# Kernel tuning notes

Hardware: AMD Instinct MI355X
Metric: run time of the kernel (lower is better)

Reference implementation:

```python
import jax, jax.numpy as jnp
import numpy as np
from jax import lax

B, CIN, COUT, K, S, P, H, W = 8, 128, 256, 3, 1, 1, 64, 64


def setup_inputs() -> dict:
    key = jax.random.key(0)
    k1, k2, k3, k4, k5 = jax.random.split(key, 5)
    fan_off = CIN * K * K
    fan_dc = CIN * K * K
    return {
        "x": jax.random.normal(k1, (B, CIN, H, W), dtype=jnp.float32),
        # offset-predicting conv: Conv2d(CIN, 2*K*K, K, S, P, padding_mode='reflect')
        "w_off": jax.random.normal(k2, (2 * K * K, CIN, K, K), dtype=jnp.float32) / np.sqrt(fan_off),
        "b_off": jax.random.normal(k3, (2 * K * K,), dtype=jnp.float32) * 0.01,
        # deformable conv weights: DeformConv2d(CIN, COUT, K, S, P)
        "w_dc": jax.random.normal(k4, (COUT, CIN, K, K), dtype=jnp.float32) / np.sqrt(fan_dc),
        "b_dc": jax.random.normal(k5, (COUT,), dtype=jnp.float32) * 0.01,
    }


def _reflect_conv(x, w, b, stride, pad):
    # Conv2d with reflect padding
    xp = jnp.pad(x, ((0, 0), (0, 0), (pad, pad), (pad, pad)), mode="reflect")
    y = lax.conv_general_dilated(xp, w, (stride, stride), "VALID",
                                 dimension_numbers=("NCHW", "OIHW", "NCHW"))
    return y + b[None, :, None, None]


def _deform_conv(x, offset, w, b, k, stride, pad):
    # torchvision DeformConv2d (v1, no mask, 1 offset group)
    Bn, C, Hi, Wi = x.shape
    Ho, Wo = offset.shape[2], offset.shape[3]
    KK = k * k
    # offset layout: [B, 2*KK, Ho, Wo], interleaved (dy, dx) per kernel position
    off = offset.reshape(Bn, KK, 2, Ho, Wo)
    hb = jnp.arange(Ho, dtype=x.dtype) * stride - pad          # base rows
    wb = jnp.arange(Wo, dtype=x.dtype) * stride - pad          # base cols
    ki, kj = jnp.meshgrid(jnp.arange(k, dtype=x.dtype), jnp.arange(k, dtype=x.dtype), indexing="ij")
    ki, kj = ki.reshape(KK), kj.reshape(KK)
    # sampling locations [B, KK, Ho, Wo]
    py = off[:, :, 0] + hb[None, None, :, None] + ki[None, :, None, None]
    px = off[:, :, 1] + wb[None, None, None, :] + kj[None, :, None, None]
    y0 = jnp.floor(py)
    x0 = jnp.floor(px)
    dy = (py - y0).reshape(Bn, 1, -1)
    dx = (px - x0).reshape(Bn, 1, -1)
    y0i = y0.astype(jnp.int32)
    x0i = x0.astype(jnp.int32)
    xf = x.reshape(Bn, C, Hi * Wi)

    def gather(yi, xi):
        valid = (yi >= 0) & (yi < Hi) & (xi >= 0) & (xi < Wi)
        yc = jnp.clip(yi, 0, Hi - 1)
        xc = jnp.clip(xi, 0, Wi - 1)
        idx = (yc * Wi + xc).reshape(Bn, -1)                   # [B, KK*Ho*Wo]
        g = jax.vmap(lambda xb, ib: xb[:, ib])(xf, idx)        # [B, C, KK*Ho*Wo]
        return g * valid.reshape(Bn, 1, -1).astype(x.dtype)

    v00 = gather(y0i, x0i)
    v01 = gather(y0i, x0i + 1)
    v10 = gather(y0i + 1, x0i)
    v11 = gather(y0i + 1, x0i + 1)
    vals = (v00 * (1 - dy) * (1 - dx) + v01 * (1 - dy) * dx
            + v10 * dy * (1 - dx) + v11 * dy * dx)             # [B, C, KK*Ho*Wo]
    cols = vals.reshape(Bn, C, KK, Ho * Wo)
    out = jnp.einsum("bckl,ock->bol", cols, w.reshape(-1, C, KK))
    out = out + b[None, :, None]
    return out.reshape(Bn, -1, Ho, Wo)


def reference(x, w_off, b_off, w_dc, b_dc):
    x_offset = _reflect_conv(x, w_off, b_off, S, P)            # [B, 2*K*K, Ho, Wo]
    # torch.chunk followed by torch.concat is an identity on the offset tensor
    return _deform_conv(x, x_offset, w_dc, b_dc, K, S, P)
```

## Files before the change

### kernel.cpp

```cpp
#include <hip/hip_runtime.h>
#include <hip/hip_fp16.h>

typedef unsigned short u16;
typedef unsigned int   u32;
typedef u32   u32x2  __attribute__((ext_vector_type(2)));
typedef u32   u32x4  __attribute__((ext_vector_type(4)));
typedef short short8 __attribute__((ext_vector_type(8)));
typedef float f32x4  __attribute__((ext_vector_type(4)));
typedef _Float16 half8 __attribute__((ext_vector_type(8)));

__device__ __forceinline__ u16 f2h(float f) { return __half_as_ushort(__float2half(f)); }
__device__ __forceinline__ f32x4 mfma16(short8 a, short8 b, f32x4 c) {
  return __builtin_amdgcn_mfma_f32_16x16x32_f16(
      __builtin_bit_cast(half8, a), __builtin_bit_cast(half8, b), c, 0, 0, 0);
}
__device__ __forceinline__ __half2 h2cast(u32 u) { return __builtin_bit_cast(__half2, u); }
__device__ __forceinline__ int refl(int v) { return v < 0 ? -v : (v > 63 ? 126 - v : v); }

__global__ __launch_bounds__(256) void prep_fused(const float* __restrict__ x,
                                                  const float* __restrict__ w_dc,
                                                  const float* __restrict__ w_off,
                                                  u16* __restrict__ xh,
                                                  u16* __restrict__ Wl2,
                                                  u16* __restrict__ Wol2) {
  int bid = blockIdx.x;
  int tid = threadIdx.x;
  if (bid < 512) {
    __shared__ float tile[128][65];
    int swz = (bid & 7) * 64 + (bid >> 3);
    int b = swz >> 6, h = swz & 63;
    for (int i = 0; i < 32; ++i) {
      int c = (tid >> 6) + i * 4;
      int w = tid & 63;
      tile[c][w] = x[(((size_t)b * 128 + c) * 64 + h) * 64 + w];
    }
    __syncthreads();
    u16* dst = xh + ((size_t)(b * 64 + h) * 64) * 128;
    for (int j = 0; j < 32; ++j) {
      int c = tid & 127;
      int w = (tid >> 7) + 2 * j;
      dst[w * 128 + c] = f2h(tile[c][w]);
    }
  } else {
    int idx = (bid - 512) * 256 + tid;
    if (idx < 294912) {
      int e = idx & 7, lane = (idx >> 3) & 63, ks = (idx >> 9) & 3;
      int mt = (idx >> 11) & 15, kk = idx >> 15;
      int o = mt * 16 + (lane & 15), c = ks * 32 + (lane >> 4) * 8 + e;
      Wl2[idx] = f2h(w_dc[(o * 128 + c) * 9 + kk]);
    } else {
      int i2 = idx - 294912;
      int e = i2 & 7, lane = (i2 >> 3) & 63, ks = (i2 >> 9) & 3;
      int mt = (i2 >> 11) & 1, kk = i2 >> 12;
      int co = mt * 16 + (lane & 15), c = ks * 32 + (lane >> 4) * 8 + e;
      Wol2[i2] = (co < 18) ? f2h(w_off[(co * 128 + c) * 9 + kk]) : (u16)0;
    }
  }
}

__device__ __forceinline__ void make_entry_lds(u32x4* __restrict__ tbl, int kk,
                                               int ho, int wo, float offy, float offx) {
  int ki = kk / 3, kj = kk - ki * 3;
  float py = offy + (float)(ho + ki - 1);
  float px = offx + (float)(wo + kj - 1);
  float fy0 = floorf(py), fx0 = floorf(px);
  int y0 = (int)fy0, x0 = (int)fx0;
  float fy = py - fy0, fx = px - fx0;
  float w11 = fy * fx, w10 = fy - w11, w01 = fx - w11, w00 = 1.f - fy - fx + w11;
  bool iy0 = (y0 >= 0) & (y0 < 64), iy1 = (y0 >= -1) & (y0 < 63);
  bool ix0 = (x0 >= 0) & (x0 < 64), ix1 = (x0 >= -1) & (x0 < 63);
  int y0c = min(max(y0, 0), 63), x0c = min(max(x0, 0), 63);
  u32 addr00 = (u32)((y0c * 64 + x0c) * 128);
  u32 dx = (x0 >= 0 && x0 < 63) ? 128u : 0u;
  u32 dy = (y0 >= 0 && y0 < 63) ? 8192u : 0u;
  u32 wA = (u32)f2h((iy0 && ix0) ? w00 : 0.f) | ((u32)f2h((iy0 && ix1) ? w01 : 0.f) << 16);
  u32 wB = (u32)f2h((iy1 && ix0) ? w10 : 0.f) | ((u32)f2h((iy1 && ix1) ? w11 : 0.f) << 16);
  u32x4 ent; ent.x = addr00; ent.y = dx | (dy << 16); ent.z = wA; ent.w = wB;
  tbl[kk * 64 + wo] = ent;
}

__global__ __launch_bounds__(512, 4) void deform_fused(
    const u16* __restrict__ xh, const u16* __restrict__ Wl2,
    const u16* __restrict__ Wol2, const float* __restrict__ b_off,
    const float* __restrict__ b_dc, float* __restrict__ out) {
  union SMU {
    u16 slab[3][64][128];
    struct { u16 cols[2][64][128]; u32x4 tbl[576]; } pb;
  };
  __shared__ SMU sm;
  int bid = blockIdx.x;
  int b = bid & 7, ho = bid >> 3;
  int tid = threadIdx.x, lane = tid & 63, wv = tid >> 6;
  int ln15 = lane & 15, kg = lane >> 4;
  const u16* xb = xh + (size_t)b * 524288;

  {
    u32x4 st[6];
#pragma unroll
    for (int i = 0; i < 6; ++i) {
      int T = tid + i * 512;
      int r = T >> 10, w = (T >> 4) & 63, cb = (T & 15) * 8;
      int hr = refl(ho + r - 1);
      st[i] = *(const u32x4*)(xb + (hr * 64 + w) * 128 + cb);
    }
#pragma unroll
    for (int i = 0; i < 6; ++i) {
      int T = tid + i * 512;
      int r = T >> 10, w = (T >> 4) & 63, cb = (T & 15) * 8;
      *(u32x4*)&sm.slab[r][w][cb ^ ((w & 7) << 3)] = st[i];
    }
  }
  __syncthreads();

  int mtA = wv & 1, ntA = wv >> 1;
  int lq = ntA * 16 + ln15;
  f32x4 oacc = {0.f, 0.f, 0.f, 0.f};
  __builtin_amdgcn_s_setprio(1);
#pragma unroll
  for (int kk = 0; kk < 9; ++kk) {
    int ki = kk / 3, kj = kk - ki * 3;
    int j = refl(lq + kj - 1);
    const u16* wb = Wol2 + ((kk * 2 + mtA) * 4) * 512 + lane * 8;
    int sbj = (j & 7) << 3;
#pragma unroll
    for (int ks = 0; ks < 4; ++ks) {
      short8 af = *(const short8*)(wb + ks * 512);
      short8 bf = *(const short8*)&sm.slab[ki][j][(ks * 32 + kg * 8) ^ sbj];
      oacc = mfma16(af, bf, oacc);
    }
  }
  __builtin_amdgcn_s_setprio(0);
  __syncthreads();

  if (mtA == 0) {
    int kkA = 2 * kg, kkB = 2 * kg + 1;
    make_entry_lds(sm.pb.tbl, kkA, ho, lq, oacc[0] + b_off[2 * kkA], oacc[1] + b_off[2 * kkA + 1]);
    make_entry_lds(sm.pb.tbl, kkB, ho, lq, oacc[2] + b_off[2 * kkB], oacc[3] + b_off[2 * kkB + 1]);
  } else if (kg == 0) {
    make_entry_lds(sm.pb.tbl, 8, ho, lq, oacc[0] + b_off[16], oacc[1] + b_off[17]);
  }
  __syncthreads();

  if (wv >= 4) {
    int pt = tid & 255;
    int tl = pt >> 4;
    int tcl = (pt & 15) * 8;
    int swzc = tcl ^ ((tl & 7) << 3);

    u32x4 gv[4][4];
    u32 gwA[4], gwB[4];
    auto gissue = [&](int g) {
#pragma unroll
      for (int i = 0; i < 4; ++i) {
        int l = tl + i * 16;
        u32x4 e = sm.pb.tbl[g * 64 + l];
        gwA[i] = e.z; gwB[i] = e.w;
        const u16* p = xb + e.x + tcl;
        u32 dxv = e.y & 0xffffu, dyv = e.y >> 16;
        gv[i][0] = *(const u32x4*)p;
        gv[i][1] = *(const u32x4*)(p + dxv);
        gv[i][2] = *(const u32x4*)(p + dyv);
        gv[i][3] = *(const u32x4*)(p + dyv + dxv);
      }
    };
    auto gwrite = [&](int dbuf) {
#pragma unroll
      for (int i = 0; i < 4; ++i) {
        int l = tl + i * 16;
        __half2 wA = h2cast(gwA[i]), wB = h2cast(gwB[i]);
        __half2 w00 = __half2half2(wA.x), w01 = __half2half2(wA.y);
        __half2 w10 = __half2half2(wB.x), w11 = __half2half2(wB.y);
        u32x4 pv;
#pragma unroll
        for (int wd = 0; wd < 4; ++wd) {
          __half2 r = __hmul2(h2cast(gv[i][0][wd]), w00);
          r = __hfma2(h2cast(gv[i][1][wd]), w01, r);
          r = __hfma2(h2cast(gv[i][2][wd]), w10, r);
          r = __hfma2(h2cast(gv[i][3][wd]), w11, r);
          pv[wd] = __builtin_bit_cast(u32, r);
        }
        *(u32x4*)&sm.pb.cols[dbuf][l][swzc] = pv;
      }
    };

    gissue(0); gwrite(0);
    gissue(1);
    __syncthreads();
    for (int kk = 0; kk < 9; ++kk) {
      int cur = kk & 1;
      if (kk < 8) gwrite(cur ^ 1);
      if (kk < 7) gissue(kk + 2);
      __syncthreads();
    }
  } else {
    f32x4 acc[4][4];
#pragma unroll
    for (int m = 0; m < 4; ++m)
#pragma unroll
      for (int n = 0; n < 4; ++n) acc[m][n] = (f32x4){0.f, 0.f, 0.f, 0.f};

    int swzb = (ln15 & 7) << 3;
    __syncthreads();
    for (int kk = 0; kk < 9; ++kk) {
      int cur = kk & 1;
      const u16* wb = Wl2 + (size_t)kk * 32768 + lane * 8;
      short8 ac[4], an[4];
#pragma unroll
      for (int m = 0; m < 4; ++m)
        ac[m] = *(const short8*)(wb + (size_t)((wv * 4 + m) * 4) * 512);
#pragma unroll
      for (int ks = 0; ks < 4; ++ks) {
        if (ks < 3) {
#pragma unroll
          for (int m = 0; m < 4; ++m)
            an[m] = *(const short8*)(wb + (size_t)((wv * 4 + m) * 4 + ks + 1) * 512);
        }
        __builtin_amdgcn_s_setprio(1);
#pragma unroll
        for (int nt = 0; nt < 4; ++nt) {
          short8 bf = *(const short8*)&sm.pb.cols[cur][nt * 16 + ln15][(ks * 32 + kg * 8) ^ swzb];
#pragma unroll
          for (int m = 0; m < 4; ++m)
            acc[m][nt] = mfma16(ac[m], bf, acc[m][nt]);
        }
        __builtin_amdgcn_s_setprio(0);
        if (ks < 3) {
#pragma unroll
          for (int m = 0; m < 4; ++m) ac[m] = an[m];
        }
      }
      __syncthreads();
    }

#pragma unroll
    for (int m = 0; m < 4; ++m) {
#pragma unroll
      for (int r = 0; r < 4; ++r) {
        int o = wv * 64 + m * 16 + kg * 4 + r;
        float bias = b_dc[o];
        size_t base = ((size_t)(b * 256 + o)) * 4096 + ho * 64;
#pragma unroll
        for (int nt = 0; nt < 4; ++nt) {
          out[base + nt * 16 + ln15] = acc[m][nt][r] + bias;
        }
      }
    }
  }
}

extern "C" void kernel_launch(void* const* d_in, const int* in_sizes, int n_in,
                              void* d_out, int out_size, void* d_ws, size_t ws_size,
                              hipStream_t stream) {
  const float* x     = (const float*)d_in[0];
  const float* w_off = (const float*)d_in[1];
  const float* b_off = (const float*)d_in[2];
  const float* w_dc  = (const float*)d_in[3];
  const float* b_dc  = (const float*)d_in[4];
  float* out = (float*)d_out;
  char* ws = (char*)d_ws;
  u16* xh   = (u16*)ws;
  u16* Wl2  = (u16*)(ws + 8388608);
  u16* Wol2 = (u16*)(ws + 8388608 + 589824);
  prep_fused  <<<dim3(1808), dim3(256), 0, stream>>>(x, w_dc, w_off, xh, Wl2, Wol2);
  deform_fused<<<dim3(512),  dim3(512), 0, stream>>>(xh, Wl2, Wol2, b_off, b_dc, out);
}
```

Baseline: 45.74 us.

## Split each output row into two 32-column halves to double block count

Each block now handles a 32-wide half of an output row instead of a full 64-wide row, so the grid doubles to 1024 blocks. The LDS slab shrinks to a 36-column halo window, the column and table buffers halve, and launch bounds ask for higher occupancy. The offset-conv MFMA work is restricted to four waves, and the GEMM drops its A-fragment prefetch and priority hints. This aims to fill more CUs and overlap more work, at the cost of reloading deform weights from global twice as often per row, plus a redundant halo load.

```diff
diff --git a/kernel.cpp b/kernel.cpp
--- a/kernel.cpp
+++ b/kernel.cpp
@@ -59,7 +59,8 @@
 }
 
 __device__ __forceinline__ void make_entry_lds(u32x4* __restrict__ tbl, int kk,
-                                               int ho, int wo, float offy, float offx) {
+                                               int ho, int wo, int lql,
+                                               float offy, float offx) {
   int ki = kk / 3, kj = kk - ki * 3;
   float py = offy + (float)(ho + ki - 1);
   float px = offx + (float)(wo + kj - 1);
@@ -76,84 +77,92 @@
   u32 wA = (u32)f2h((iy0 && ix0) ? w00 : 0.f) | ((u32)f2h((iy0 && ix1) ? w01 : 0.f) << 16);
   u32 wB = (u32)f2h((iy1 && ix0) ? w10 : 0.f) | ((u32)f2h((iy1 && ix1) ? w11 : 0.f) << 16);
   u32x4 ent; ent.x = addr00; ent.y = dx | (dy << 16); ent.z = wA; ent.w = wB;
-  tbl[kk * 64 + wo] = ent;
-}
-
-__global__ __launch_bounds__(512, 4) void deform_fused(
+  tbl[kk * 32 + lql] = ent;
+}
+
+__global__ __launch_bounds__(512, 8) void deform_fused(
     const u16* __restrict__ xh, const u16* __restrict__ Wl2,
     const u16* __restrict__ Wol2, const float* __restrict__ b_off,
     const float* __restrict__ b_dc, float* __restrict__ out) {
-  union SMU {
-    u16 slab[3][64][128];
-    struct { u16 cols[2][64][128]; u32x4 tbl[576]; } pb;
-  };
-  __shared__ SMU sm;
+  __shared__ union SMU {
+    u16 slab[3][36][128];
+    u16 cols[2][32][128];
+  } sm;
+  __shared__ u32x4 tbl[288];
+
   int bid = blockIdx.x;
-  int b = bid & 7, ho = bid >> 3;
+  int b = bid & 7;
+  int ho = (bid >> 3) & 63;
+  int l0 = (bid >> 9) * 32;
   int tid = threadIdx.x, lane = tid & 63, wv = tid >> 6;
   int ln15 = lane & 15, kg = lane >> 4;
   const u16* xb = xh + (size_t)b * 524288;
 
   {
-    u32x4 st[6];
-#pragma unroll
-    for (int i = 0; i < 6; ++i) {
+    u32x4 st[4];
+#pragma unroll
+    for (int i = 0; i < 4; ++i) {
       int T = tid + i * 512;
-      int r = T >> 10, w = (T >> 4) & 63, cb = (T & 15) * 8;
-      int hr = refl(ho + r - 1);
-      st[i] = *(const u32x4*)(xb + (hr * 64 + w) * 128 + cb);
-    }
-#pragma unroll
-    for (int i = 0; i < 6; ++i) {
+      if (T < 1728) {
+        int r = T / 576, rem = T - r * 576;
+        int j = rem >> 4, cb = (rem & 15) * 8;
+        int hr = refl(ho + r - 1);
+        int w = refl(l0 + j - 1);
+        st[i] = *(const u32x4*)(xb + (hr * 64 + w) * 128 + cb);
+      }
+    }
+#pragma unroll
+    for (int i = 0; i < 4; ++i) {
       int T = tid + i * 512;
-      int r = T >> 10, w = (T >> 4) & 63, cb = (T & 15) * 8;
-      *(u32x4*)&sm.slab[r][w][cb ^ ((w & 7) << 3)] = st[i];
+      if (T < 1728) {
+        int r = T / 576, rem = T - r * 576;
+        int j = rem >> 4, cb = (rem & 15) * 8;
+        *(u32x4*)&sm.slab[r][j][cb ^ ((j & 7) << 3)] = st[i];
+      }
     }
   }
   __syncthreads();
 
-  int mtA = wv & 1, ntA = wv >> 1;
-  int lq = ntA * 16 + ln15;
-  f32x4 oacc = {0.f, 0.f, 0.f, 0.f};
-  __builtin_amdgcn_s_setprio(1);
-#pragma unroll
-  for (int kk = 0; kk < 9; ++kk) {
-    int ki = kk / 3, kj = kk - ki * 3;
-    int j = refl(lq + kj - 1);
-    const u16* wb = Wol2 + ((kk * 2 + mtA) * 4) * 512 + lane * 8;
-    int sbj = (j & 7) << 3;
-#pragma unroll
-    for (int ks = 0; ks < 4; ++ks) {
-      short8 af = *(const short8*)(wb + ks * 512);
-      short8 bf = *(const short8*)&sm.slab[ki][j][(ks * 32 + kg * 8) ^ sbj];
-      oacc = mfma16(af, bf, oacc);
-    }
-  }
-  __builtin_amdgcn_s_setprio(0);
-  __syncthreads();
-
-  if (mtA == 0) {
-    int kkA = 2 * kg, kkB = 2 * kg + 1;
-    make_entry_lds(sm.pb.tbl, kkA, ho, lq, oacc[0] + b_off[2 * kkA], oacc[1] + b_off[2 * kkA + 1]);
-    make_entry_lds(sm.pb.tbl, kkB, ho, lq, oacc[2] + b_off[2 * kkB], oacc[3] + b_off[2 * kkB + 1]);
-  } else if (kg == 0) {
-    make_entry_lds(sm.pb.tbl, 8, ho, lq, oacc[0] + b_off[16], oacc[1] + b_off[17]);
+  if (wv < 4) {
+    int mtA = wv & 1, ntq = wv >> 1;
+    int lql = ntq * 16 + ln15;
+    f32x4 oacc = {0.f, 0.f, 0.f, 0.f};
+#pragma unroll
+    for (int kk = 0; kk < 9; ++kk) {
+      int ki = kk / 3, kj = kk - ki * 3;
+      int j = lql + kj;
+      int sbj = (j & 7) << 3;
+      const u16* wb = Wol2 + ((kk * 2 + mtA) * 4) * 512 + lane * 8;
+#pragma unroll
+      for (int ks = 0; ks < 4; ++ks) {
+        short8 af = *(const short8*)(wb + ks * 512);
+        short8 bf = *(const short8*)&sm.slab[ki][j][(ks * 32 + kg * 8) ^ sbj];
+        oacc = mfma16(af, bf, oacc);
+      }
+    }
+    if (mtA == 0) {
+      int kkA = 2 * kg, kkB = 2 * kg + 1;
+      make_entry_lds(tbl, kkA, ho, l0 + lql, lql, oacc[0] + b_off[2 * kkA], oacc[1] + b_off[2 * kkA + 1]);
+      make_entry_lds(tbl, kkB, ho, l0 + lql, lql, oacc[2] + b_off[2 * kkB], oacc[3] + b_off[2 * kkB + 1]);
+    } else if (kg == 0) {
+      make_entry_lds(tbl, 8, ho, l0 + lql, lql, oacc[0] + b_off[16], oacc[1] + b_off[17]);
+    }
   }
   __syncthreads();
 
   if (wv >= 4) {
     int pt = tid & 255;
-    int tl = pt >> 4;
+    int tl0 = pt >> 4;
     int tcl = (pt & 15) * 8;
-    int swzc = tcl ^ ((tl & 7) << 3);
-
-    u32x4 gv[4][4];
-    u32 gwA[4], gwB[4];
+    int swzc = tcl ^ ((tl0 & 7) << 3);
+
+    u32x4 gv[2][4];
+    u32 gwA[2], gwB[2];
     auto gissue = [&](int g) {
 #pragma unroll
-      for (int i = 0; i < 4; ++i) {
-        int l = tl + i * 16;
-        u32x4 e = sm.pb.tbl[g * 64 + l];
+      for (int i = 0; i < 2; ++i) {
+        int l = tl0 + i * 16;
+        u32x4 e = tbl[g * 32 + l];
         gwA[i] = e.z; gwB[i] = e.w;
         const u16* p = xb + e.x + tcl;
         u32 dxv = e.y & 0xffffu, dyv = e.y >> 16;
@@ -165,8 +174,8 @@
     };
     auto gwrite = [&](int dbuf) {
 #pragma unroll
-      for (int i = 0; i < 4; ++i) {
-        int l = tl + i * 16;
+      for (int i = 0; i < 2; ++i) {
+        int l = tl0 + i * 16;
         __half2 wA = h2cast(gwA[i]), wB = h2cast(gwB[i]);
         __half2 w00 = __half2half2(wA.x), w01 = __half2half2(wA.y);
         __half2 w10 = __half2half2(wB.x), w11 = __half2half2(wB.y);
@@ -179,7 +188,7 @@
           r = __hfma2(h2cast(gv[i][3][wd]), w11, r);
           pv[wd] = __builtin_bit_cast(u32, r);
         }
-        *(u32x4*)&sm.pb.cols[dbuf][l][swzc] = pv;
+        *(u32x4*)&sm.cols[dbuf][l][swzc] = pv;
       }
     };
 
@@ -193,41 +202,31 @@
       __syncthreads();
     }
   } else {
-    f32x4 acc[4][4];
-#pragma unroll
-    for (int m = 0; m < 4; ++m)
-#pragma unroll
-      for (int n = 0; n < 4; ++n) acc[m][n] = (f32x4){0.f, 0.f, 0.f, 0.f};
-
+    int cg = wv;
+    f32x4 acc[4][2];
+#pragma unroll
+    for (int m = 0; m < 4; ++m) {
+      acc[m][0] = (f32x4){0.f, 0.f, 0.f, 0.f};
+      acc[m][1] = (f32x4){0.f, 0.f, 0.f, 0.f};
+    }
     int swzb = (ln15 & 7) << 3;
     __syncthreads();
     for (int kk = 0; kk < 9; ++kk) {
       int cur = kk & 1;
       const u16* wb = Wl2 + (size_t)kk * 32768 + lane * 8;
-      short8 ac[4], an[4];
-#pragma unroll
-      for (int m = 0; m < 4; ++m)
-        ac[m] = *(const short8*)(wb + (size_t)((wv * 4 + m) * 4) * 512);
 #pragma unroll
       for (int ks = 0; ks < 4; ++ks) {
-        if (ks < 3) {
+        short8 a[4];
+#pragma unroll
+        for (int m = 0; m < 4; ++m)
+          a[m] = *(const short8*)(wb + (size_t)((cg * 4 + m) * 4 + ks) * 512);
+#pragma unroll
+        for (int nt = 0; nt < 2; ++nt) {
+          short8 bf = *(const short8*)&sm.cols[cur][nt * 16 + ln15][(ks * 32 + kg * 8) ^ swzb];
 #pragma unroll
           for (int m = 0; m < 4; ++m)
-            an[m] = *(const short8*)(wb + (size_t)((wv * 4 + m) * 4 + ks + 1) * 512);
+            acc[m][nt] = mfma16(a[m], bf, acc[m][nt]);
         }
-        __builtin_amdgcn_s_setprio(1);
-#pragma unroll
-        for (int nt = 0; nt < 4; ++nt) {
-          short8 bf = *(const short8*)&sm.pb.cols[cur][nt * 16 + ln15][(ks * 32 + kg * 8) ^ swzb];
-#pragma unroll
-          for (int m = 0; m < 4; ++m)
-            acc[m][nt] = mfma16(ac[m], bf, acc[m][nt]);
-        }
-        __builtin_amdgcn_s_setprio(0);
-        if (ks < 3) {
-#pragma unroll
-          for (int m = 0; m < 4; ++m) ac[m] = an[m];
-        }
       }
       __syncthreads();
     }
@@ -236,13 +235,11 @@
     for (int m = 0; m < 4; ++m) {
 #pragma unroll
       for (int r = 0; r < 4; ++r) {
-        int o = wv * 64 + m * 16 + kg * 4 + r;
+        int o = cg * 64 + m * 16 + kg * 4 + r;
         float bias = b_dc[o];
-        size_t base = ((size_t)(b * 256 + o)) * 4096 + ho * 64;
-#pragma unroll
-        for (int nt = 0; nt < 4; ++nt) {
-          out[base + nt * 16 + ln15] = acc[m][nt][r] + bias;
-        }
+        size_t base = ((size_t)(b * 256 + o)) * 4096 + ho * 64 + l0;
+        out[base + ln15]      = acc[m][0][r] + bias;
+        out[base + 16 + ln15] = acc[m][1][r] + bias;
       }
     }
   }
@@ -262,5 +259,5 @@
   u16* Wl2  = (u16*)(ws + 8388608);
   u16* Wol2 = (u16*)(ws + 8388608 + 589824);
   prep_fused  <<<dim3(1808), dim3(256), 0, stream>>>(x, w_dc, w_off, xh, Wl2, Wol2);
-  deform_fused<<<dim3(512),  dim3(512), 0, stream>>>(xh, Wl2, Wol2, b_off, b_dc, out);
-}
+  deform_fused<<<dim3(1024), dim3(512), 0, stream>>>(xh, Wl2, Wol2, b_off, b_dc, out);
+}
```

Result: slower. 109.1 us (+138.5%).
